# Performance work log

Measured on AMD Instinct MI355X. Metric: run time of the kernel, lower is better.

Reference implementation:

```python
import jax, jax.numpy as jnp
import numpy as np
from jax import lax

B = 128; LEADS = 12; T = 1000; DM = 128; DI = 256; DS = 16; DR = 8; DC = 4; NB = 4; L = 199; OUT = 256


def _ln(x, g, b):
    m = x.mean(-1, keepdims=True)
    v = ((x - m) ** 2).mean(-1, keepdims=True)
    return (x - m) * lax.rsqrt(v + 1e-5) * g + b


def _ssm_scan(u, delta, A, Bm, Cm, D):
    """Selective scan. u, delta: [B,L,DI]; Bm, Cm: [B,L,DS]; A: [DI,DS]; D: [DI]."""
    def step(h, inp):
        d_t, B_t, C_t, u_t = inp  # [B,DI],[B,DS],[B,DS],[B,DI]
        dA = jnp.exp(d_t[:, :, None] * A[None])            # [B,DI,DS]
        h = dA * h + (d_t * u_t)[:, :, None] * B_t[:, None, :]
        y = jnp.einsum('bds,bs->bd', h, C_t)
        return h, y
    h0 = jnp.zeros((u.shape[0], A.shape[0], A.shape[1]), u.dtype)
    xs = (jnp.moveaxis(delta, 1, 0), jnp.moveaxis(Bm, 1, 0),
          jnp.moveaxis(Cm, 1, 0), jnp.moveaxis(u, 1, 0))
    _, ys = lax.scan(step, h0, xs)
    return jnp.moveaxis(ys, 0, 1) + u * D[None, None, :]


def setup_inputs() -> dict:
    key = jax.random.key(0)
    ks = jax.random.split(key, 16)
    n = lambda k, shp, s: jax.random.normal(k, shp, jnp.float32) * s
    inp = {}
    inp['x'] = jax.random.normal(ks[0], (B, LEADS, T), jnp.float32)
    inp['pe_w'] = n(ks[1], (DM, LEADS, 10), 0.1)
    inp['pe_b'] = jnp.zeros((DM,), jnp.float32)
    inp['gn_g'] = jnp.ones((DM,), jnp.float32)
    inp['gn_b'] = jnp.zeros((DM,), jnp.float32)
    inp['pos'] = n(ks[2], (1, L, DM), 0.02)
    inp['ln1_g'] = jnp.ones((NB, DM), jnp.float32)
    inp['ln1_b'] = jnp.zeros((NB, DM), jnp.float32)
    inp['in_w'] = n(ks[3], (NB, 2 * DI, DM), 0.05)
    inp['conv_w'] = n(ks[4], (NB, DI, DC), 0.2)
    inp['conv_b'] = jnp.zeros((NB, DI), jnp.float32)
    inp['xproj_w'] = n(ks[5], (NB, DR + 2 * DS, DI), 0.05)
    inp['dtproj_w'] = n(ks[6], (NB, DI, DR), 0.2)
    inp['dtproj_b'] = jnp.full((NB, DI), -4.6, jnp.float32)  # softplus(-4.6) ~= 0.01
    inp['A_log'] = jnp.tile(jnp.log(jnp.arange(1, DS + 1, dtype=jnp.float32))[None, None, :], (NB, DI, 1))
    inp['Dp'] = jnp.ones((NB, DI), jnp.float32)
    inp['outw'] = n(ks[7], (NB, DM, DI), 0.05)
    inp['ln2_g'] = jnp.ones((NB, DM), jnp.float32)
    inp['ln2_b'] = jnp.zeros((NB, DM), jnp.float32)
    inp['ffn_w1'] = n(ks[8], (NB, 4 * DM, DM), 0.05)
    inp['ffn_b1'] = jnp.zeros((NB, 4 * DM), jnp.float32)
    inp['ffn_w2'] = n(ks[9], (NB, DM, 4 * DM), 0.05)
    inp['ffn_b2'] = jnp.zeros((NB, DM), jnp.float32)
    inp['lnf_g'] = jnp.ones((DM,), jnp.float32)
    inp['lnf_b'] = jnp.zeros((DM,), jnp.float32)
    inp['head_w'] = n(ks[10], (OUT, DM), 0.05)
    inp['head_b'] = jnp.zeros((OUT,), jnp.float32)
    return inp


def reference(x, pe_w, pe_b, gn_g, gn_b, pos, ln1_g, ln1_b, in_w, conv_w, conv_b,
              xproj_w, dtproj_w, dtproj_b, A_log, Dp, outw, ln2_g, ln2_b,
              ffn_w1, ffn_b1, ffn_w2, ffn_b2, lnf_g, lnf_b, head_w, head_b):
    # --- patch embed: Conv1d(12 -> DM, k=10, s=5) + GroupNorm(8) + GELU ---
    h = lax.conv_general_dilated(x, pe_w, (5,), 'VALID',
                                 dimension_numbers=('NCH', 'OIH', 'NCH'))
    h = h + pe_b[None, :, None]                      # [B, DM, L]
    Bb, _, Lc = h.shape
    hg = h.reshape(Bb, 8, DM // 8, Lc)
    m = hg.mean((2, 3), keepdims=True)
    v = ((hg - m) ** 2).mean((2, 3), keepdims=True)
    h = ((hg - m) * lax.rsqrt(v + 1e-5)).reshape(Bb, DM, Lc)
    h = h * gn_g[None, :, None] + gn_b[None, :, None]
    h = jax.nn.gelu(h, approximate=False)
    h = jnp.swapaxes(h, 1, 2) + pos                  # [B, L, DM]

    for i in range(NB):
        # --- Mamba block ---
        u = _ln(h, ln1_g[i], ln1_b[i])
        xz = u @ in_w[i].T                           # [B, L, 2*DI]
        xm, z = jnp.split(xz, 2, axis=-1)
        xc = jnp.swapaxes(xm, 1, 2)                  # [B, DI, L]
        xc = jnp.pad(xc, ((0, 0), (0, 0), (DC - 1, 0)))  # causal pad
        xc = lax.conv_general_dilated(xc, conv_w[i][:, None, :], (1,), 'VALID',
                                      dimension_numbers=('NCH', 'OIH', 'NCH'),
                                      feature_group_count=DI)
        xc = xc + conv_b[i][None, :, None]
        u_ssm = jax.nn.silu(jnp.swapaxes(xc, 1, 2))  # [B, L, DI]
        dbl = u_ssm @ xproj_w[i].T                   # [B, L, DR+2*DS]
        dt, Bm, Cm = dbl[..., :DR], dbl[..., DR:DR + DS], dbl[..., DR + DS:]
        delta = jax.nn.softplus(dt @ dtproj_w[i].T + dtproj_b[i])  # [B, L, DI]
        A = -jnp.exp(A_log[i])                       # [DI, DS]
        y = _ssm_scan(u_ssm, delta, A, Bm, Cm, Dp[i])
        y = y * jax.nn.silu(z)
        h = h + y @ outw[i].T
        # --- FFN block ---
        f = _ln(h, ln2_g[i], ln2_b[i])
        f = jax.nn.gelu(f @ ffn_w1[i].T + ffn_b1[i], approximate=False)
        h = h + f @ ffn_w2[i].T + ffn_b2[i]

    h = _ln(h, lnf_g, lnf_b).mean(axis=1)            # [B, DM]
    return jax.nn.gelu(h @ head_w.T + head_b, approximate=False)  # [B, OUT]
```

## Files before the change

kernel.cpp:

```cpp
#include <hip/hip_runtime.h>
#include <math.h>

#define TOKS (128*199)
#define DM 128
#define DI 256
#define DS 16
#define DR 8
#define NBLK 4
#define LSEQ 199
#define BATCH 128

typedef __attribute__((ext_vector_type(8))) short bf16x8;
typedef __attribute__((ext_vector_type(4))) float f32x4;

__device__ __forceinline__ float gelu_f(float x) {
  return 0.5f * x * (1.0f + erff(x * 0.70710678118654752440f));
}
__device__ __forceinline__ float silu_fast(float x) {
  float e = __expf(-x);
  return x * __builtin_amdgcn_rcpf(1.0f + e);
}
__device__ __forceinline__ unsigned short f2bf(float f) {
  unsigned u = __float_as_uint(f);
  u += 0x7fffu + ((u >> 16) & 1u);
  return (unsigned short)(u >> 16);
}
__device__ __forceinline__ float bf2f(unsigned short h) {
  return __uint_as_float(((unsigned)h) << 16);
}

__global__ __launch_bounds__(256) void cvtw_kernel(const float* __restrict__ src,
                                                   unsigned short* __restrict__ dh,
                                                   unsigned short* __restrict__ dl, int n) {
  int i = blockIdx.x*256 + threadIdx.x;
  if (i < n) {
    float v = src[i];
    unsigned short h = f2bf(v);
    dh[i] = h;
    dl[i] = f2bf(v - bf2f(h));
  }
}
__global__ __launch_bounds__(256) void cvtw_pad_kernel(const float* __restrict__ src,
                                                       unsigned short* __restrict__ dh,
                                                       unsigned short* __restrict__ dl) {
  int i = blockIdx.x*256 + threadIdx.x;
  int blk = i >> 14, rem = i & 16383;
  int r = rem >> 8, c = rem & 255;
  float v = (r < 40) ? src[(size_t)blk*40*256 + r*256 + c] : 0.f;
  unsigned short h = f2bf(v);
  dh[i] = h;
  dl[i] = f2bf(v - bf2f(h));
}

__global__ __launch_bounds__(256) void pe_conv_kernel(
    const float* __restrict__ x, const float* __restrict__ pw,
    const float* __restrict__ pb, float* __restrict__ convo) {
  int b = blockIdx.x, tc = blockIdx.y;
  int t0 = tc * 25;
  int nt = (LSEQ - t0 < 25) ? (LSEQ - t0) : 25;
  __shared__ float sx[12][136];
  int tid = threadIdx.x;
  for (int i = tid; i < 12*136; i += 256) {
    int l = i / 136, k = i - l*136;
    int idx = t0*5 + k;
    sx[l][k] = (idx < 1000) ? x[(size_t)b*12000 + l*1000 + idx] : 0.f;
  }
  __syncthreads();
  for (int o = tid; o < DM*nt; o += 256) {
    int m = o / nt, tt = o - m*nt;
    const float* wr = pw + m*120;
    float acc = pb[m];
#pragma unroll
    for (int l = 0; l < 12; ++l) {
#pragma unroll
      for (int k = 0; k < 10; ++k)
        acc += sx[l][tt*5 + k] * wr[l*10 + k];
    }
    convo[((size_t)b*DM + m)*LSEQ + t0 + tt] = acc;
  }
}

__global__ void gn_kernel(const float* __restrict__ conv, const float* __restrict__ gg,
                          const float* __restrict__ gb, const float* __restrict__ pos,
                          float* __restrict__ h) {
  int b = blockIdx.x >> 3, grp = blockIdx.x & 7;
  const float* cb = conv + ((size_t)b*DM + grp*16)*LSEQ;
  int tid = threadIdx.x;
  float s = 0.f, s2 = 0.f;
  for (int i = tid; i < 16*LSEQ; i += 256) { float v = cb[i]; s += v; s2 += v*v; }
#pragma unroll
  for (int m = 1; m < 64; m <<= 1) { s += __shfl_xor(s, m); s2 += __shfl_xor(s2, m); }
  __shared__ float red[8];
  int lane = tid & 63, wid = tid >> 6;
  if (lane == 0) { red[wid] = s; red[4+wid] = s2; }
  __syncthreads();
  float S  = red[0]+red[1]+red[2]+red[3];
  float S2 = red[4]+red[5]+red[6]+red[7];
  const float inv = 1.0f/(16.0f*LSEQ);
  float mean = S*inv;
  float var  = S2*inv - mean*mean;
  float rstd = rsqrtf(var + 1e-5f);
  for (int i = tid; i < 16*LSEQ; i += 256) {
    int mloc = i / LSEQ; int t = i - mloc*LSEQ;
    int m = grp*16 + mloc;
    float v = (cb[i] - mean)*rstd*gg[m] + gb[m];
    v = gelu_f(v);
    h[((size_t)b*LSEQ + t)*DM + m] = v + pos[t*DM + m];
  }
}

__global__ void ln_kernel(const float* __restrict__ x, const float* __restrict__ g,
                          const float* __restrict__ bb,
                          unsigned short* __restrict__ oh, unsigned short* __restrict__ ol) {
  int tok = blockIdx.x*4 + (threadIdx.x >> 6);
  int lane = threadIdx.x & 63;
  const float* xr = x + (size_t)tok*DM;
  float v0 = xr[lane], v1 = xr[lane+64];
  float s = v0+v1, s2 = v0*v0+v1*v1;
#pragma unroll
  for (int m=1;m<64;m<<=1){ s += __shfl_xor(s,m); s2 += __shfl_xor(s2,m); }
  float mean = s*(1.f/DM);
  float var  = s2*(1.f/DM) - mean*mean;
  float rs = rsqrtf(var+1e-5f);
  float y0 = (v0-mean)*rs*g[lane]+bb[lane];
  float y1 = (v1-mean)*rs*g[lane+64]+bb[lane+64];
  size_t o0 = (size_t)tok*DM + lane;
  unsigned short h0 = f2bf(y0), h1 = f2bf(y1);
  oh[o0]    = h0; ol[o0]    = f2bf(y0 - bf2f(h0));
  oh[o0+64] = h1; ol[o0+64] = f2bf(y1 - bf2f(h1));
}

template<int MODE, int BIAS>
__global__ __launch_bounds__(256) void gemm_bf(
    const unsigned short* __restrict__ Ah, const unsigned short* __restrict__ Al,
    const unsigned short* __restrict__ Wh, const unsigned short* __restrict__ Wl,
    const float* __restrict__ bias,
    float* __restrict__ Cf, unsigned short* __restrict__ Ch, unsigned short* __restrict__ Cl,
    float* __restrict__ Cf2, int N, int K) {
  __shared__ unsigned short sAh[64*32], sAl[64*32], sWh[64*32], sWl[64*32];
  int tid = threadIdx.x;
  int w = tid >> 6, l = tid & 63;
  int fr = l & 15, fq = l >> 4;
  int srow = tid >> 2, sseg = tid & 3;
  const unsigned short* pAh = Ah + (size_t)(blockIdx.x*64 + srow)*K + sseg*8;
  const unsigned short* pAl = Al + (size_t)(blockIdx.x*64 + srow)*K + sseg*8;
  const unsigned short* pWh = Wh + (size_t)(blockIdx.y*64 + srow)*K + sseg*8;
  const unsigned short* pWl = Wl + (size_t)(blockIdx.y*64 + srow)*K + sseg*8;
  f32x4 acc[4];
#pragma unroll
  for (int ns=0;ns<4;++ns) acc[ns] = (f32x4){0.f,0.f,0.f,0.f};
  uint4 vah = *(const uint4*)pAh;
  uint4 val_ = *(const uint4*)pAl;
  uint4 vwh = *(const uint4*)pWh;
  uint4 vwl = *(const uint4*)pWl;
  int sidx = srow*32 + sseg*8;
  for (int k0 = 0; k0 < K; k0 += 32) {
    __syncthreads();
    *(uint4*)&sAh[sidx] = vah;
    *(uint4*)&sAl[sidx] = val_;
    *(uint4*)&sWh[sidx] = vwh;
    *(uint4*)&sWl[sidx] = vwl;
    __syncthreads();
    if (k0 + 32 < K) {
      vah = *(const uint4*)(pAh + k0 + 32);
      val_ = *(const uint4*)(pAl + k0 + 32);
      vwh = *(const uint4*)(pWh + k0 + 32);
      vwl = *(const uint4*)(pWl + k0 + 32);
    }
    bf16x8 ah = *(const bf16x8*)&sAh[(w*16+fr)*32 + fq*8];
    bf16x8 al = *(const bf16x8*)&sAl[(w*16+fr)*32 + fq*8];
#pragma unroll
    for (int ns=0;ns<4;++ns) {
      bf16x8 wh = *(const bf16x8*)&sWh[(ns*16+fr)*32 + fq*8];
      bf16x8 wl = *(const bf16x8*)&sWl[(ns*16+fr)*32 + fq*8];
      acc[ns] = __builtin_amdgcn_mfma_f32_16x16x32_bf16(ah, wh, acc[ns], 0, 0, 0);
      acc[ns] = __builtin_amdgcn_mfma_f32_16x16x32_bf16(al, wh, acc[ns], 0, 0, 0);
      acc[ns] = __builtin_amdgcn_mfma_f32_16x16x32_bf16(ah, wl, acc[ns], 0, 0, 0);
    }
  }
  int row0 = blockIdx.x*64 + w*16 + fq*4;
#pragma unroll
  for (int ns=0;ns<4;++ns) {
    int col = blockIdx.y*64 + ns*16 + fr;
    float bv = BIAS ? bias[col] : 0.f;
#pragma unroll
    for (int v=0;v<4;++v) {
      float val = acc[ns][v] + bv;
      size_t row = (size_t)(row0 + v);
      if (MODE == 0) {
        Cf[row*N + col] = val;
      } else if (MODE == 1) {
        Cf[row*N + col] += val;
      } else if (MODE == 2) {
        val = gelu_f(val);
        unsigned short hh = f2bf(val);
        Ch[row*N + col] = hh;
        Cl[row*N + col] = f2bf(val - bf2f(hh));
      } else {
        if (col < 256) Cf[row*256 + col] = val;
        else           Cf2[row*256 + (col-256)] = val;
      }
    }
  }
}

__global__ void dwconv_kernel(const float* __restrict__ X, const float* __restrict__ w,
                              const float* __restrict__ bias, float* __restrict__ uss,
                              unsigned short* __restrict__ ussh, unsigned short* __restrict__ ussl) {
  int tok = blockIdx.x;
  int d = threadIdx.x;
  int t = tok % LSEQ;
  float4 wv = *(const float4*)(w + d*4);
  float acc = bias[d];
  const float* xp = X + (size_t)tok*DI + d;
  if (t >= 3) acc += xp[-3*DI]*wv.x;
  if (t >= 2) acc += xp[-2*DI]*wv.y;
  if (t >= 1) acc += xp[-1*DI]*wv.z;
  acc += xp[0]*wv.w;
  float sv = silu_fast(acc);
  size_t o = (size_t)tok*DI + d;
  uss[o] = sv;
  unsigned short hh = f2bf(sv);
  ussh[o] = hh;
  ussl[o] = f2bf(sv - bf2f(hh));
}

__global__ __launch_bounds__(256) void dtproj_kernel(
    const float* __restrict__ dbl, const float* __restrict__ dtw,
    const float* __restrict__ dtb, float* __restrict__ dlt) {
  int tok0 = blockIdx.x * 8;
  int d = threadIdx.x;
  __shared__ float sdt[8][DR];
  if (d < 64) sdt[d >> 3][d & 7] = dbl[(size_t)(tok0 + (d >> 3))*64 + (d & 7)];
  float wreg[DR];
#pragma unroll
  for (int rr = 0; rr < DR; ++rr) wreg[rr] = dtw[d*DR + rr];
  float b0 = dtb[d];
  __syncthreads();
#pragma unroll
  for (int tt = 0; tt < 8; ++tt) {
    float acc = b0;
#pragma unroll
    for (int rr = 0; rr < DR; ++rr) acc += sdt[tt][rr]*wreg[rr];
    acc = (acc > 20.f) ? acc : log1pf(__expf(acc));
    dlt[(size_t)(tok0 + tt)*DI + d] = acc;
  }
}

__global__ __launch_bounds__(256) void scan_kernel(
    const float* __restrict__ uss, const float* __restrict__ dlt,
    const float* __restrict__ dbl,
    const float* __restrict__ A_log, const float* __restrict__ Dp,
    const float* __restrict__ Z,
    unsigned short* __restrict__ yh, unsigned short* __restrict__ yl) {
  int bg = blockIdx.x;
  int b = bg >> 4, dg = bg & 15;
  int tid = threadIdx.x;
  int s = tid & 15, dloc = tid >> 4;
  int d = dg*16 + dloc;
  float As = -__expf(A_log[d*DS + s]);
  float Dd = Dp[d];
  float h = 0.f;
  size_t tokbase = (size_t)b*LSEQ;
  const float* pdt = dlt + tokbase*DI + d;
  const float* pu  = uss + tokbase*DI + d;
  const float* pz  = Z   + tokbase*DI + d;
  const float* pB  = dbl + tokbase*64 + 8  + s;
  const float* pC  = dbl + tokbase*64 + 24 + s;
  size_t ooff = tokbase*DI + d;
  float dt_c = *pdt, u_c = *pu, z_c = *pz, B_c = *pB, C_c = *pC;
  for (int t = 0; t < LSEQ; ++t) {
    float dt = dt_c, u = u_c, z = z_c, Bv = B_c, Cv = C_c;
    if (t + 1 < LSEQ) {
      pdt += DI; pu += DI; pz += DI; pB += 64; pC += 64;
      dt_c = *pdt; u_c = *pu; z_c = *pz; B_c = *pB; C_c = *pC;
    }
    float dA = __expf(dt*As);
    h = fmaf(dA, h, dt*u*Bv);
    float p = h*Cv;
    p += __shfl_xor(p, 1);
    p += __shfl_xor(p, 2);
    p += __shfl_xor(p, 4);
    p += __shfl_xor(p, 8);
    if (s == 0) {
      float yv = fmaf(u, Dd, p) * silu_fast(z);
      unsigned short hh = f2bf(yv);
      yh[ooff] = hh;
      yl[ooff] = f2bf(yv - bf2f(hh));
    }
    ooff += DI;
  }
}

__global__ void final_kernel(const float* __restrict__ h, const float* __restrict__ g,
                             const float* __restrict__ bta, const float* __restrict__ hw,
                             const float* __restrict__ hb, float* __restrict__ out) {
  int b = blockIdx.x;
  int tid = threadIdx.x, lane = tid & 63, wid = tid >> 6;
  float s0 = 0.f, s1 = 0.f;
  for (int t = wid; t < LSEQ; t += 4) {
    const float* hr = h + ((size_t)b*LSEQ + t)*DM;
    float v0 = hr[lane], v1 = hr[lane+64];
    float ss = v0+v1, ss2 = v0*v0+v1*v1;
#pragma unroll
    for (int m=1;m<64;m<<=1){ ss += __shfl_xor(ss,m); ss2 += __shfl_xor(ss2,m); }
    float mean = ss*(1.f/DM);
    float var  = ss2*(1.f/DM)-mean*mean;
    float rs = rsqrtf(var+1e-5f);
    s0 += (v0-mean)*rs*g[lane]+bta[lane];
    s1 += (v1-mean)*rs*g[lane+64]+bta[lane+64];
  }
  __shared__ float sm[4][128];
  sm[wid][lane] = s0; sm[wid][lane+64] = s1;
  __syncthreads();
  __shared__ float mv[128];
  if (tid < 128) mv[tid] = (sm[0][tid]+sm[1][tid]+sm[2][tid]+sm[3][tid]) * (1.f/199.f);
  __syncthreads();
  int j = tid;
  const float* wr = hw + (size_t)j*DM;
  float acc = hb[j];
#pragma unroll 4
  for (int k=0;k<DM;k++) acc += mv[k]*wr[k];
  out[(size_t)b*256 + j] = gelu_f(acc);
}

extern "C" void kernel_launch(void* const* d_in, const int* in_sizes, int n_in,
                              void* d_out, int out_size, void* d_ws, size_t ws_size,
                              hipStream_t stream) {
  const float* x       = (const float*)d_in[0];
  const float* pe_w    = (const float*)d_in[1];
  const float* pe_b    = (const float*)d_in[2];
  const float* gn_g    = (const float*)d_in[3];
  const float* gn_b    = (const float*)d_in[4];
  const float* pos     = (const float*)d_in[5];
  const float* ln1_g   = (const float*)d_in[6];
  const float* ln1_b   = (const float*)d_in[7];
  const float* in_w    = (const float*)d_in[8];
  const float* conv_w  = (const float*)d_in[9];
  const float* conv_b  = (const float*)d_in[10];
  const float* xproj_w = (const float*)d_in[11];
  const float* dtproj_w= (const float*)d_in[12];
  const float* dtproj_b= (const float*)d_in[13];
  const float* A_log   = (const float*)d_in[14];
  const float* Dp      = (const float*)d_in[15];
  const float* outw    = (const float*)d_in[16];
  const float* ln2_g   = (const float*)d_in[17];
  const float* ln2_b   = (const float*)d_in[18];
  const float* ffn_w1  = (const float*)d_in[19];
  const float* ffn_b1  = (const float*)d_in[20];
  const float* ffn_w2  = (const float*)d_in[21];
  const float* ffn_b2  = (const float*)d_in[22];
  const float* lnf_g   = (const float*)d_in[23];
  const float* lnf_b   = (const float*)d_in[24];
  const float* head_w  = (const float*)d_in[25];
  const float* head_b  = (const float*)d_in[26];
  float* out = (float*)d_out;

  float* ws  = (float*)d_ws;
  float* h    = ws;
  float* X    = h   + (size_t)TOKS*DM;
  float* Z    = X   + (size_t)TOKS*DI;
  float* uss  = Z   + (size_t)TOKS*DI;
  float* dlt  = uss + (size_t)TOKS*DI;
  float* dbl  = dlt + (size_t)TOKS*DI;
  unsigned short* uh   = (unsigned short*)(dbl + (size_t)TOKS*64);
  unsigned short* ul   = uh   + (size_t)TOKS*DM;
  unsigned short* ussh = ul   + (size_t)TOKS*DM;
  unsigned short* ussl = ussh + (size_t)TOKS*DI;
  unsigned short* wb   = ussl + (size_t)TOKS*DI;
  unsigned short* inwh = wb;
  unsigned short* inwl = inwh + 262144;
  unsigned short* xpwh = inwl + 262144;
  unsigned short* xpwl = xpwh + 65536;
  unsigned short* outwh= xpwl + 65536;
  unsigned short* outwl= outwh + 131072;
  unsigned short* w1h  = outwl + 131072;
  unsigned short* w1l  = w1h + 262144;
  unsigned short* w2h  = w1l + 262144;
  unsigned short* w2l  = w2h + 262144;
  unsigned short* yh   = (unsigned short*)X;
  unsigned short* yl   = yh + (size_t)TOKS*DI;
  unsigned short* f1h  = (unsigned short*)uss;
  unsigned short* f1l  = f1h + (size_t)TOKS*512;

  cvtw_kernel<<<1024, 256, 0, stream>>>(in_w,   inwh, inwl, 262144);
  cvtw_pad_kernel<<<256, 256, 0, stream>>>(xproj_w, xpwh, xpwl);
  cvtw_kernel<<<512, 256, 0, stream>>>(outw,   outwh, outwl, 131072);
  cvtw_kernel<<<1024, 256, 0, stream>>>(ffn_w1, w1h, w1l, 262144);
  cvtw_kernel<<<1024, 256, 0, stream>>>(ffn_w2, w2h, w2l, 262144);

  pe_conv_kernel<<<dim3(BATCH, 8), 256, 0, stream>>>(x, pe_w, pe_b, X);
  gn_kernel<<<BATCH*8, 256, 0, stream>>>(X, gn_g, gn_b, pos, h);

  for (int i = 0; i < NBLK; ++i) {
    ln_kernel<<<TOKS/4, 256, 0, stream>>>(h, ln1_g + i*DM, ln1_b + i*DM, uh, ul);
    gemm_bf<3,0><<<dim3(TOKS/64, 8), 256, 0, stream>>>(
        uh, ul, inwh + (size_t)i*65536, inwl + (size_t)i*65536,
        nullptr, X, nullptr, nullptr, Z, 512, DM);
    dwconv_kernel<<<TOKS, 256, 0, stream>>>(X, conv_w + i*DI*4, conv_b + i*DI,
                                            uss, ussh, ussl);
    gemm_bf<0,0><<<dim3(TOKS/64, 1), 256, 0, stream>>>(
        ussh, ussl, xpwh + (size_t)i*16384, xpwl + (size_t)i*16384,
        nullptr, dbl, nullptr, nullptr, nullptr, 64, DI);
    dtproj_kernel<<<TOKS/8, 256, 0, stream>>>(
        dbl, dtproj_w + (size_t)i*DI*DR, dtproj_b + i*DI, dlt);
    scan_kernel<<<BATCH*16, 256, 0, stream>>>(
        uss, dlt, dbl, A_log + (size_t)i*DI*DS, Dp + i*DI, Z, yh, yl);
    gemm_bf<1,0><<<dim3(TOKS/64, 2), 256, 0, stream>>>(
        yh, yl, outwh + (size_t)i*32768, outwl + (size_t)i*32768,
        nullptr, h, nullptr, nullptr, nullptr, DM, DI);
    ln_kernel<<<TOKS/4, 256, 0, stream>>>(h, ln2_g + i*DM, ln2_b + i*DM, uh, ul);
    gemm_bf<2,1><<<dim3(TOKS/64, 8), 256, 0, stream>>>(
        uh, ul, w1h + (size_t)i*65536, w1l + (size_t)i*65536,
        ffn_b1 + i*512, nullptr, f1h, f1l, nullptr, 512, DM);
    gemm_bf<1,1><<<dim3(TOKS/64, 2), 256, 0, stream>>>(
        f1h, f1l, w2h + (size_t)i*65536, w2l + (size_t)i*65536,
        ffn_b2 + i*DM, h, nullptr, nullptr, nullptr, DM, 512);
  }

  final_kernel<<<BATCH, 256, 0, stream>>>(h, lnf_g, lnf_b, head_w, head_b, out);
}
```

Before: 1.392 ms.

## Double-buffer GEMM tiles with direct global-to-LDS loads and 128-row blocks

Replaces the split-bf16 GEMM with a version that computes a 128x64 output tile per block, so each wave does two M sub-tiles and reuses its W fragments across them. Tile data goes straight from global memory to LDS with global_load_lds into two alternating buffers, which removes the register staging and one barrier per k-step. An XOR swizzle on the k-segment is meant to cut LDS bank conflicts. In exchange the grid has half as many blocks and each block uses more LDS and accumulator registers. The code relies on the barrier also waiting for the asynchronous LDS loads to finish.

```diff
diff --git a/kernel.cpp b/kernel.cpp
--- a/kernel.cpp
+++ b/kernel.cpp
@@ -131,74 +131,96 @@
 }
 
 template<int MODE, int BIAS>
-__global__ __launch_bounds__(256) void gemm_bf(
+__global__ __launch_bounds__(256) void gemm_bf2(
     const unsigned short* __restrict__ Ah, const unsigned short* __restrict__ Al,
     const unsigned short* __restrict__ Wh, const unsigned short* __restrict__ Wl,
     const float* __restrict__ bias,
     float* __restrict__ Cf, unsigned short* __restrict__ Ch, unsigned short* __restrict__ Cl,
     float* __restrict__ Cf2, int N, int K) {
-  __shared__ unsigned short sAh[64*32], sAl[64*32], sWh[64*32], sWl[64*32];
-  int tid = threadIdx.x;
-  int w = tid >> 6, l = tid & 63;
-  int fr = l & 15, fq = l >> 4;
-  int srow = tid >> 2, sseg = tid & 3;
-  const unsigned short* pAh = Ah + (size_t)(blockIdx.x*64 + srow)*K + sseg*8;
-  const unsigned short* pAl = Al + (size_t)(blockIdx.x*64 + srow)*K + sseg*8;
-  const unsigned short* pWh = Wh + (size_t)(blockIdx.y*64 + srow)*K + sseg*8;
-  const unsigned short* pWl = Wl + (size_t)(blockIdx.y*64 + srow)*K + sseg*8;
-  f32x4 acc[4];
-#pragma unroll
-  for (int ns=0;ns<4;++ns) acc[ns] = (f32x4){0.f,0.f,0.f,0.f};
-  uint4 vah = *(const uint4*)pAh;
-  uint4 val_ = *(const uint4*)pAl;
-  uint4 vwh = *(const uint4*)pWh;
-  uint4 vwl = *(const uint4*)pWl;
-  int sidx = srow*32 + sseg*8;
+  __shared__ unsigned short lds[2][12288];
+  const int tid = threadIdx.x;
+  const int w = tid >> 6, l = tid & 63;
+  const int fr = l & 15, fq = l >> 4;
+  const int frsw = (fr >> 1) & 3;
+  const int crow = l >> 2;
+  const int ksl = (l & 3) ^ ((l >> 3) & 3);
+  const size_t bm0 = (size_t)blockIdx.x * 128;
+  const size_t bn0 = (size_t)blockIdx.y * 64;
+
+  const unsigned short* gAh0 = Ah + (bm0 + (size_t)(w*16 + crow))*K + ksl*8;
+  const unsigned short* gAh1 = Ah + (bm0 + (size_t)((w+4)*16 + crow))*K + ksl*8;
+  const unsigned short* gAl0 = Al + (bm0 + (size_t)(w*16 + crow))*K + ksl*8;
+  const unsigned short* gAl1 = Al + (bm0 + (size_t)((w+4)*16 + crow))*K + ksl*8;
+  const unsigned short* gWh0 = Wh + (bn0 + (size_t)(w*16 + crow))*K + ksl*8;
+  const unsigned short* gWl0 = Wl + (bn0 + (size_t)(w*16 + crow))*K + ksl*8;
+
+  f32x4 acc[2][4];
+#pragma unroll
+  for (int mi=0;mi<2;++mi)
+#pragma unroll
+    for (int ns=0;ns<4;++ns) acc[mi][ns] = (f32x4){0.f,0.f,0.f,0.f};
+
+#define STAGE(BUF, KO) do { \
+    unsigned short* bb_ = lds[BUF]; \
+    __builtin_amdgcn_global_load_lds(gAh0 + (KO), &bb_[w*512],          16, 0, 0); \
+    __builtin_amdgcn_global_load_lds(gAh1 + (KO), &bb_[(w+4)*512],      16, 0, 0); \
+    __builtin_amdgcn_global_load_lds(gAl0 + (KO), &bb_[4096 + w*512],   16, 0, 0); \
+    __builtin_amdgcn_global_load_lds(gAl1 + (KO), &bb_[4096 + (w+4)*512], 16, 0, 0); \
+    __builtin_amdgcn_global_load_lds(gWh0 + (KO), &bb_[8192 + w*512],   16, 0, 0); \
+    __builtin_amdgcn_global_load_lds(gWl0 + (KO), &bb_[10240 + w*512],  16, 0, 0); \
+  } while (0)
+
+  int cur = 0;
+  STAGE(0, 0);
   for (int k0 = 0; k0 < K; k0 += 32) {
     __syncthreads();
-    *(uint4*)&sAh[sidx] = vah;
-    *(uint4*)&sAl[sidx] = val_;
-    *(uint4*)&sWh[sidx] = vwh;
-    *(uint4*)&sWl[sidx] = vwl;
-    __syncthreads();
-    if (k0 + 32 < K) {
-      vah = *(const uint4*)(pAh + k0 + 32);
-      val_ = *(const uint4*)(pAl + k0 + 32);
-      vwh = *(const uint4*)(pWh + k0 + 32);
-      vwl = *(const uint4*)(pWl + k0 + 32);
-    }
-    bf16x8 ah = *(const bf16x8*)&sAh[(w*16+fr)*32 + fq*8];
-    bf16x8 al = *(const bf16x8*)&sAl[(w*16+fr)*32 + fq*8];
+    if (k0 + 32 < K) STAGE(cur ^ 1, k0 + 32);
+    const unsigned short* b = lds[cur];
+    bf16x8 whf[4], wlf[4];
 #pragma unroll
     for (int ns=0;ns<4;++ns) {
-      bf16x8 wh = *(const bf16x8*)&sWh[(ns*16+fr)*32 + fq*8];
-      bf16x8 wl = *(const bf16x8*)&sWl[(ns*16+fr)*32 + fq*8];
-      acc[ns] = __builtin_amdgcn_mfma_f32_16x16x32_bf16(ah, wh, acc[ns], 0, 0, 0);
-      acc[ns] = __builtin_amdgcn_mfma_f32_16x16x32_bf16(al, wh, acc[ns], 0, 0, 0);
-      acc[ns] = __builtin_amdgcn_mfma_f32_16x16x32_bf16(ah, wl, acc[ns], 0, 0, 0);
-    }
-  }
-  int row0 = blockIdx.x*64 + w*16 + fq*4;
-#pragma unroll
-  for (int ns=0;ns<4;++ns) {
-    int col = blockIdx.y*64 + ns*16 + fr;
-    float bv = BIAS ? bias[col] : 0.f;
-#pragma unroll
-    for (int v=0;v<4;++v) {
-      float val = acc[ns][v] + bv;
-      size_t row = (size_t)(row0 + v);
-      if (MODE == 0) {
-        Cf[row*N + col] = val;
-      } else if (MODE == 1) {
-        Cf[row*N + col] += val;
-      } else if (MODE == 2) {
-        val = gelu_f(val);
-        unsigned short hh = f2bf(val);
-        Ch[row*N + col] = hh;
-        Cl[row*N + col] = f2bf(val - bf2f(hh));
-      } else {
-        if (col < 256) Cf[row*256 + col] = val;
-        else           Cf2[row*256 + (col-256)] = val;
+      whf[ns] = *(const bf16x8*)&b[ 8192 + (ns*16 + fr)*32 + ((fq^frsw)*8)];
+      wlf[ns] = *(const bf16x8*)&b[10240 + (ns*16 + fr)*32 + ((fq^frsw)*8)];
+    }
+#pragma unroll
+    for (int mi=0;mi<2;++mi) {
+      bf16x8 ah = *(const bf16x8*)&b[       (w*32 + mi*16 + fr)*32 + ((fq^frsw)*8)];
+      bf16x8 al = *(const bf16x8*)&b[4096 + (w*32 + mi*16 + fr)*32 + ((fq^frsw)*8)];
+#pragma unroll
+      for (int ns=0;ns<4;++ns) {
+        acc[mi][ns] = __builtin_amdgcn_mfma_f32_16x16x32_bf16(ah, whf[ns], acc[mi][ns], 0, 0, 0);
+        acc[mi][ns] = __builtin_amdgcn_mfma_f32_16x16x32_bf16(al, whf[ns], acc[mi][ns], 0, 0, 0);
+        acc[mi][ns] = __builtin_amdgcn_mfma_f32_16x16x32_bf16(ah, wlf[ns], acc[mi][ns], 0, 0, 0);
+      }
+    }
+    cur ^= 1;
+  }
+#undef STAGE
+
+  const int row0 = (int)bm0 + w*32;
+#pragma unroll
+  for (int mi=0;mi<2;++mi) {
+#pragma unroll
+    for (int ns=0;ns<4;++ns) {
+      int col = (int)bn0 + ns*16 + fr;
+      float bv = BIAS ? bias[col] : 0.f;
+#pragma unroll
+      for (int v=0;v<4;++v) {
+        float val = acc[mi][ns][v] + bv;
+        size_t row = (size_t)(row0 + mi*16 + fq*4 + v);
+        if (MODE == 0) {
+          Cf[row*N + col] = val;
+        } else if (MODE == 1) {
+          Cf[row*N + col] += val;
+        } else if (MODE == 2) {
+          val = gelu_f(val);
+          unsigned short hh = f2bf(val);
+          Ch[row*N + col] = hh;
+          Cl[row*N + col] = f2bf(val - bf2f(hh));
+        } else {
+          if (col < 256) Cf[row*256 + col] = val;
+          else           Cf2[row*256 + (col-256)] = val;
+        }
       }
     }
   }
@@ -394,26 +416,26 @@
 
   for (int i = 0; i < NBLK; ++i) {
     ln_kernel<<<TOKS/4, 256, 0, stream>>>(h, ln1_g + i*DM, ln1_b + i*DM, uh, ul);
-    gemm_bf<3,0><<<dim3(TOKS/64, 8), 256, 0, stream>>>(
+    gemm_bf2<3,0><<<dim3(TOKS/128, 8), 256, 0, stream>>>(
         uh, ul, inwh + (size_t)i*65536, inwl + (size_t)i*65536,
         nullptr, X, nullptr, nullptr, Z, 512, DM);
     dwconv_kernel<<<TOKS, 256, 0, stream>>>(X, conv_w + i*DI*4, conv_b + i*DI,
                                             uss, ussh, ussl);
-    gemm_bf<0,0><<<dim3(TOKS/64, 1), 256, 0, stream>>>(
+    gemm_bf2<0,0><<<dim3(TOKS/128, 1), 256, 0, stream>>>(
         ussh, ussl, xpwh + (size_t)i*16384, xpwl + (size_t)i*16384,
         nullptr, dbl, nullptr, nullptr, nullptr, 64, DI);
     dtproj_kernel<<<TOKS/8, 256, 0, stream>>>(
         dbl, dtproj_w + (size_t)i*DI*DR, dtproj_b + i*DI, dlt);
     scan_kernel<<<BATCH*16, 256, 0, stream>>>(
         uss, dlt, dbl, A_log + (size_t)i*DI*DS, Dp + i*DI, Z, yh, yl);
-    gemm_bf<1,0><<<dim3(TOKS/64, 2), 256, 0, stream>>>(
+    gemm_bf2<1,0><<<dim3(TOKS/128, 2), 256, 0, stream>>>(
         yh, yl, outwh + (size_t)i*32768, outwl + (size_t)i*32768,
         nullptr, h, nullptr, nullptr, nullptr, DM, DI);
     ln_kernel<<<TOKS/4, 256, 0, stream>>>(h, ln2_g + i*DM, ln2_b + i*DM, uh, ul);
-    gemm_bf<2,1><<<dim3(TOKS/64, 8), 256, 0, stream>>>(
+    gemm_bf2<2,1><<<dim3(TOKS/128, 8), 256, 0, stream>>>(
         uh, ul, w1h + (size_t)i*65536, w1l + (size_t)i*65536,
         ffn_b1 + i*512, nullptr, f1h, f1l, nullptr, 512, DM);
-    gemm_bf<1,1><<<dim3(TOKS/64, 2), 256, 0, stream>>>(
+    gemm_bf2<1,1><<<dim3(TOKS/128, 2), 256, 0, stream>>>(
         f1h, f1l, w2h + (size_t)i*65536, w2l + (size_t)i*65536,
         ffn_b2 + i*DM, h, nullptr, nullptr, nullptr, DM, 512);
   }
```

New measurement: 1.408 ms. No clear change (+1.1%).
